# Performance work log

Hardware: AMD Instinct MI355X
Metric: run time of the kernel (lower is better)

Reference implementation:

```python
import jax, jax.numpy as jnp
import numpy as np

NUM_HEADS = 12
HEAD_DIM = 64
SCALE = HEAD_DIM ** -0.5


def setup_inputs() -> dict:
    key = jax.random.key(0)
    ks = jax.random.split(key, 5)
    B, N, C = 8, 1024, 768
    x = jax.random.normal(ks[0], (B, N, C), dtype=jnp.float32)
    qkv_w = jax.random.normal(ks[1], (3 * C, C), dtype=jnp.float32) * (C ** -0.5)
    qkv_b = jax.random.normal(ks[2], (3 * C,), dtype=jnp.float32) * 0.02
    proj_w = jax.random.normal(ks[3], (C, C), dtype=jnp.float32) * (C ** -0.5)
    proj_b = jax.random.normal(ks[4], (C,), dtype=jnp.float32) * 0.02
    return {"x": x, "qkv_w": qkv_w, "qkv_b": qkv_b, "proj_w": proj_w, "proj_b": proj_b}


def reference(x, qkv_w, qkv_b, proj_w, proj_b):
    B, N, C = x.shape
    H, D = NUM_HEADS, HEAD_DIM
    # qkv projection: (B,N,3C) -> (3,B,H,N,D)
    qkv = (x @ qkv_w.T + qkv_b).reshape(B, N, 3, H, D).transpose(2, 0, 3, 1, 4)
    q, k, v = qkv[0], qkv[1], qkv[2]
    q = q * SCALE
    # full N x N attention scores, softmax over keys
    attn = jax.nn.softmax(jnp.einsum("bhnd,bhmd->bhnm", q, k), axis=-1)
    # Libragrad: detach the softmax map before multiplying with V
    attn = jax.lax.stop_gradient(attn)
    out = jnp.einsum("bhnm,bhmd->bhnd", attn, v)  # (B,H,N,D)
    out = out.transpose(0, 2, 1, 3).reshape(B, N, C)
    return out @ proj_w.T + proj_b
```

## Files before the change

kernel.cpp:

```cpp
#include <hip/hip_runtime.h>

#define NH 12
#define HD 64
#define BB 8
#define SEQ 1024
#define CD 768

typedef __bf16 bf16x8 __attribute__((ext_vector_type(8)));
typedef float f32x4 __attribute__((ext_vector_type(4)));

__device__ __forceinline__ unsigned short f2bf(float f) {
    unsigned int u = __float_as_uint(f);
    u = (u + 0x7fffu + ((u >> 16) & 1u)) >> 16;
    return (unsigned short)u;
}

__device__ __forceinline__ void gld_lds16(const unsigned short* g, unsigned short* l) {
    __builtin_amdgcn_global_load_lds(
        (const __attribute__((address_space(1))) unsigned int*)g,
        (__attribute__((address_space(3))) unsigned int*)l, 16, 0, 0);
}

__device__ __forceinline__ int slot2key(int s) {
    return (s & 3) + 4 * ((s >> 3) & 3) + 16 * ((s >> 2) & 1) + 32 * (s >> 5);
}

#define N4_X 1572864
#define N4_W1 442368
#define N4_W2 147456
__global__ void cast_all(const float* __restrict__ x, const float* __restrict__ w1,
                         const float* __restrict__ w2,
                         unsigned short* __restrict__ ox, unsigned short* __restrict__ ow1,
                         unsigned short* __restrict__ ow2) {
    int i = blockIdx.x * blockDim.x + threadIdx.x;
    const float4* src;
    ushort4* dst;
    if (i < N4_X) {
        src = (const float4*)x + i; dst = (ushort4*)ox + i;
    } else if (i < N4_X + N4_W1) {
        src = (const float4*)w1 + (i - N4_X); dst = (ushort4*)ow1 + (i - N4_X);
    } else if (i < N4_X + N4_W1 + N4_W2) {
        src = (const float4*)w2 + (i - N4_X - N4_W1); dst = (ushort4*)ow2 + (i - N4_X - N4_W1);
    } else return;
    float4 f = *src;
    ushort4 o;
    o.x = f2bf(f.x); o.y = f2bf(f.y); o.z = f2bf(f.z); o.w = f2bf(f.w);
    *dst = o;
}

template<int MODE>
__global__ __launch_bounds__(256)
void gemm_bt(const unsigned short* __restrict__ A, const unsigned short* __restrict__ W,
             const float* __restrict__ bias,
             unsigned short* __restrict__ qb, unsigned short* __restrict__ kb,
             unsigned short* __restrict__ vb, float* __restrict__ fout,
             int M, int N, int K) {
    __shared__ __attribute__((aligned(16))) unsigned short As[128 * 32];
    __shared__ __attribute__((aligned(16))) unsigned short Bs[128 * 32];

    const int t    = threadIdx.x;
    const int bm0  = blockIdx.x * 128;
    const int bn0  = blockIdx.y * 128;
    const int wave = t >> 6;
    const int lane = t & 63;
    const int wm   = (wave >> 1) * 64;
    const int wn   = (wave & 1) * 64;
    const int col  = lane & 15;
    const int quad = lane >> 4;

    const int srow = t >> 2;
    const int scol = (t & 3) * 8;

    f32x4 acc[4][4];
#pragma unroll
    for (int i = 0; i < 4; i++)
#pragma unroll
        for (int j = 0; j < 4; j++) acc[i][j] = (f32x4){0.f, 0.f, 0.f, 0.f};

    for (int k0 = 0; k0 < K; k0 += 32) {
        __syncthreads();
        gld_lds16(A + (size_t)(bm0 + srow) * K + k0 + scol,      As + srow * 32 + scol);
        gld_lds16(A + (size_t)(bm0 + 64 + srow) * K + k0 + scol, As + (64 + srow) * 32 + scol);
        gld_lds16(W + (size_t)(bn0 + srow) * K + k0 + scol,      Bs + srow * 32 + scol);
        gld_lds16(W + (size_t)(bn0 + 64 + srow) * K + k0 + scol, Bs + (64 + srow) * 32 + scol);
        __syncthreads();

        bf16x8 af[4], bf[4];
#pragma unroll
        for (int mi = 0; mi < 4; mi++)
            af[mi] = *(const bf16x8*)(As + (wm + mi * 16 + col) * 32 + quad * 8);
#pragma unroll
        for (int ni = 0; ni < 4; ni++)
            bf[ni] = *(const bf16x8*)(Bs + (wn + ni * 16 + col) * 32 + quad * 8);
#pragma unroll
        for (int mi = 0; mi < 4; mi++)
#pragma unroll
            for (int ni = 0; ni < 4; ni++)
                acc[mi][ni] = __builtin_amdgcn_mfma_f32_16x16x32_bf16(
                    af[mi], bf[ni], acc[mi][ni], 0, 0, 0);
    }

    if (MODE == 1) {
#pragma unroll
        for (int mi = 0; mi < 4; mi++)
#pragma unroll
            for (int ni = 0; ni < 4; ni++) {
                const int n = bn0 + wn + ni * 16 + col;
                const float bv = bias[n];
#pragma unroll
                for (int r = 0; r < 4; r++) {
                    const int m = bm0 + wm + mi * 16 + quad * 4 + r;
                    fout[(size_t)m * N + n] = acc[mi][ni][r] + bv;
                }
            }
        return;
    }

    const int sel = bn0 / 768;
    const int nb  = bn0 - sel * 768;
    const int b   = bm0 >> 10;
    const int nqb = bm0 & 1023;
    unsigned short* const dstbuf = (sel == 0) ? qb : (sel == 1) ? kb : vb;
    const float scale = (sel == 0) ? 0.18033688f : 1.0f;

#pragma unroll
    for (int ni = 0; ni < 4; ni++) {
        const int hn = nb + wn + ni * 16;
        const int h  = hn >> 6;
        const int d0 = hn & 63;
        const float bv = bias[bn0 + wn + ni * 16 + col];
        unsigned short* const rowbase =
            dstbuf + ((size_t)(b * NH + h) * SEQ) * HD + d0 + col;
#pragma unroll
        for (int mi = 0; mi < 4; mi++)
#pragma unroll
            for (int r = 0; r < 4; r++) {
                const int nq = nqb + wm + mi * 16 + quad * 4 + r;
                rowbase[(size_t)nq * HD] = f2bf((acc[mi][ni][r] + bv) * scale);
            }
    }
}

__global__ __launch_bounds__(256)
void vtrans(const unsigned short* __restrict__ v, unsigned short* __restrict__ vt) {
    __shared__ __attribute__((aligned(16))) unsigned short T[64 * 72];
    const int bh = blockIdx.x;
    const int kt = blockIdx.y;
    const int t  = threadIdx.x;
    const int r  = t >> 2;
    const int c  = (t & 3) * 16;

    const unsigned short* src = v + ((size_t)bh * SEQ + kt * 64 + r) * HD + c;
    *(uint4*)(T + r * 72 + c)     = *(const uint4*)src;
    *(uint4*)(T + r * 72 + c + 8) = *(const uint4*)(src + 8);
    __syncthreads();

    union { unsigned short us[16]; uint4 u4[2]; } o;
#pragma unroll
    for (int j = 0; j < 16; j++) o.us[j] = T[slot2key(c + j) * 72 + r];
    unsigned short* dst = vt + ((size_t)bh * HD + r) * SEQ + kt * 64 + c;
    *(uint4*)dst       = o.u4[0];
    *(uint4*)(dst + 8) = o.u4[1];
}

__global__ __launch_bounds__(256, 6)
void attn_mfma(const unsigned short* __restrict__ qb,
               const unsigned short* __restrict__ kb,
               const unsigned short* __restrict__ vb,
               unsigned short* __restrict__ ob) {
    __shared__ __attribute__((aligned(16))) unsigned short Ks[64 * 72];
    __shared__ __attribute__((aligned(16))) unsigned short VT[64 * 72];

    const int t  = threadIdx.x;
    const int bh = blockIdx.x;
    const int qt = blockIdx.y;
    const size_t base = (size_t)bh * SEQ * HD;

    const int sr = t >> 2;
    const int sc = (t & 3) * 16;

    const int wave = t >> 6;
    const int lane = t & 63;
    const int col  = lane & 15;
    const int quad = lane >> 4;

    bf16x8 aq0, aq1;
    {
        const int q = qt * 64 + wave * 16 + col;
        aq0 = *(const bf16x8*)(qb + base + (size_t)q * HD + quad * 8);
        aq1 = *(const bf16x8*)(qb + base + (size_t)q * HD + 32 + quad * 8);
    }

    float l_r = 0.f;
    f32x4 accO[4];
#pragma unroll
    for (int di = 0; di < 4; di++) accO[di] = (f32x4){0.f, 0.f, 0.f, 0.f};

    const unsigned short* kp = kb + base + (size_t)sr * HD + sc;
    const unsigned short* vp = vb + base + (size_t)sr * SEQ + sc;
    uint4 kr0 = *(const uint4*)kp,  kr1 = *(const uint4*)(kp + 8);
    uint4 vr0 = *(const uint4*)vp,  vr1 = *(const uint4*)(vp + 8);

    for (int kc = 0; kc < 16; kc++) {
        __syncthreads();
        *(uint4*)(Ks + sr * 72 + sc)     = kr0;
        *(uint4*)(Ks + sr * 72 + sc + 8) = kr1;
        *(uint4*)(VT + sr * 72 + sc)     = vr0;
        *(uint4*)(VT + sr * 72 + sc + 8) = vr1;
        __syncthreads();

        if (kc < 15) {
            const unsigned short* kn = kp + (size_t)(kc + 1) * 64 * HD;
            const unsigned short* vn = vp + (size_t)(kc + 1) * 64;
            kr0 = *(const uint4*)kn; kr1 = *(const uint4*)(kn + 8);
            vr0 = *(const uint4*)vn; vr1 = *(const uint4*)(vn + 8);
        }

        f32x4 accT[4];
        __builtin_amdgcn_s_setprio(1);
#pragma unroll
        for (int ni = 0; ni < 4; ni++) {
            bf16x8 bk0 = *(const bf16x8*)(Ks + (ni * 16 + col) * 72 + quad * 8);
            bf16x8 bk1 = *(const bf16x8*)(Ks + (ni * 16 + col) * 72 + 32 + quad * 8);
            f32x4 z = (f32x4){0.f, 0.f, 0.f, 0.f};
            z = __builtin_amdgcn_mfma_f32_16x16x32_bf16(bk0, aq0, z, 0, 0, 0);
            z = __builtin_amdgcn_mfma_f32_16x16x32_bf16(bk1, aq1, z, 0, 0, 0);
            accT[ni] = z;
        }
        __builtin_amdgcn_s_setprio(0);

        union { __bf16 b[16]; bf16x8 v[2]; } apu;
#pragma unroll
        for (int ni = 0; ni < 4; ni++) {
            float p0 = __builtin_exp2f(accT[ni][0]);
            float p1 = __builtin_exp2f(accT[ni][1]);
            float p2 = __builtin_exp2f(accT[ni][2]);
            float p3 = __builtin_exp2f(accT[ni][3]);
            l_r += (p0 + p1) + (p2 + p3);
            apu.b[ni * 4 + 0] = (__bf16)p0;
            apu.b[ni * 4 + 1] = (__bf16)p1;
            apu.b[ni * 4 + 2] = (__bf16)p2;
            apu.b[ni * 4 + 3] = (__bf16)p3;
        }

        __builtin_amdgcn_s_setprio(1);
#pragma unroll
        for (int di = 0; di < 4; di++) {
            bf16x8 bv0 = *(const bf16x8*)(VT + (di * 16 + col) * 72 + quad * 8);
            bf16x8 bv1 = *(const bf16x8*)(VT + (di * 16 + col) * 72 + 32 + quad * 8);
            accO[di] = __builtin_amdgcn_mfma_f32_16x16x32_bf16(apu.v[0], bv0, accO[di], 0, 0, 0);
            accO[di] = __builtin_amdgcn_mfma_f32_16x16x32_bf16(apu.v[1], bv1, accO[di], 0, 0, 0);
        }
        __builtin_amdgcn_s_setprio(0);
    }

    const int b = bh / NH, h = bh - b * NH;
    float s = l_r;
    s += __shfl_xor(s, 16);
    s += __shfl_xor(s, 32);
#pragma unroll
    for (int r = 0; r < 4; r++) {
        const float inv = 1.f / __shfl(s, quad * 4 + r);
        const int q = qt * 64 + wave * 16 + quad * 4 + r;
        const size_t rowbase = ((size_t)b * SEQ + q) * CD + h * 64;
#pragma unroll
        for (int di = 0; di < 4; di++)
            ob[rowbase + di * 16 + col] = f2bf(accO[di][r] * inv);
    }
}

extern "C" void kernel_launch(void* const* d_in, const int* in_sizes, int n_in,
                              void* d_out, int out_size, void* d_ws, size_t ws_size,
                              hipStream_t stream) {
    const float* x      = (const float*)d_in[0];
    const float* qkv_w  = (const float*)d_in[1];
    const float* qkv_b  = (const float*)d_in[2];
    const float* proj_w = (const float*)d_in[3];
    const float* proj_b = (const float*)d_in[4];
    float* out = (float*)d_out;

    char* ws = (char*)d_ws;
    unsigned short* x_bf     = (unsigned short*)ws;
    unsigned short* qkvw_bf  = (unsigned short*)(ws + 12582912);
    unsigned short* projw_bf = (unsigned short*)(ws + 12582912 + 3538944);
    unsigned short* q_bf     = (unsigned short*)(ws + 12582912 + 3538944 + 1179648);
    unsigned short* k_bf     = q_bf + 6291456;
    unsigned short* v_bf     = k_bf + 6291456;
    unsigned short* vt_bf    = x_bf;
    unsigned short* attn_bf  = v_bf;

    cast_all<<<8448, 256, 0, stream>>>(x, qkv_w, proj_w, x_bf, qkvw_bf, projw_bf);

    gemm_bt<0><<<dim3(64, 18), 256, 0, stream>>>(x_bf, qkvw_bf, qkv_b,
                                                 q_bf, k_bf, v_bf, nullptr,
                                                 8192, 2304, 768);

    vtrans<<<dim3(96, 16), 256, 0, stream>>>(v_bf, vt_bf);

    attn_mfma<<<dim3(96, 16), 256, 0, stream>>>(q_bf, k_bf, vt_bf, attn_bf);

    gemm_bt<1><<<dim3(64, 6), 256, 0, stream>>>(attn_bf, projw_bf, proj_b,
                                                nullptr, nullptr, nullptr, out,
                                                8192, 768, 768);
}
```

Before: 213.1 us.

## Double-buffer K/V shared tiles in attention kernel to drop one barrier

```diff
diff --git a/kernel.cpp b/kernel.cpp
--- a/kernel.cpp
+++ b/kernel.cpp
@@ -163,13 +163,13 @@
     *(uint4*)(dst + 8) = o.u4[1];
 }
 
-__global__ __launch_bounds__(256, 6)
+__global__ __launch_bounds__(256, 4)
 void attn_mfma(const unsigned short* __restrict__ qb,
                const unsigned short* __restrict__ kb,
                const unsigned short* __restrict__ vb,
                unsigned short* __restrict__ ob) {
-    __shared__ __attribute__((aligned(16))) unsigned short Ks[64 * 72];
-    __shared__ __attribute__((aligned(16))) unsigned short VT[64 * 72];
+    __shared__ __attribute__((aligned(16))) unsigned short Ks[2][64 * 72];
+    __shared__ __attribute__((aligned(16))) unsigned short VT[2][64 * 72];
 
     const int t  = threadIdx.x;
     const int bh = blockIdx.x;
@@ -198,20 +198,29 @@
 
     const unsigned short* kp = kb + base + (size_t)sr * HD + sc;
     const unsigned short* vp = vb + base + (size_t)sr * SEQ + sc;
+    const int so = sr * 72 + sc;
+
     uint4 kr0 = *(const uint4*)kp,  kr1 = *(const uint4*)(kp + 8);
     uint4 vr0 = *(const uint4*)vp,  vr1 = *(const uint4*)(vp + 8);
-
-    for (int kc = 0; kc < 16; kc++) {
+    *(uint4*)(Ks[0] + so)     = kr0;
+    *(uint4*)(Ks[0] + so + 8) = kr1;
+    *(uint4*)(VT[0] + so)     = vr0;
+    *(uint4*)(VT[0] + so + 8) = vr1;
+    kr0 = *(const uint4*)(kp + 64 * HD);  kr1 = *(const uint4*)(kp + 64 * HD + 8);
+    vr0 = *(const uint4*)(vp + 64);       vr1 = *(const uint4*)(vp + 64 + 8);
+
+    auto chunk = [&](int kc, const unsigned short* Kc, const unsigned short* Vc,
+                     unsigned short* Kn, unsigned short* Vn) {
         __syncthreads();
-        *(uint4*)(Ks + sr * 72 + sc)     = kr0;
-        *(uint4*)(Ks + sr * 72 + sc + 8) = kr1;
-        *(uint4*)(VT + sr * 72 + sc)     = vr0;
-        *(uint4*)(VT + sr * 72 + sc + 8) = vr1;
-        __syncthreads();
-
         if (kc < 15) {
-            const unsigned short* kn = kp + (size_t)(kc + 1) * 64 * HD;
-            const unsigned short* vn = vp + (size_t)(kc + 1) * 64;
+            *(uint4*)(Kn + so)     = kr0;
+            *(uint4*)(Kn + so + 8) = kr1;
+            *(uint4*)(Vn + so)     = vr0;
+            *(uint4*)(Vn + so + 8) = vr1;
+        }
+        if (kc < 14) {
+            const unsigned short* kn = kp + (size_t)(kc + 2) * 64 * HD;
+            const unsigned short* vn = vp + (size_t)(kc + 2) * 64;
             kr0 = *(const uint4*)kn; kr1 = *(const uint4*)(kn + 8);
             vr0 = *(const uint4*)vn; vr1 = *(const uint4*)(vn + 8);
         }
@@ -220,8 +229,8 @@
         __builtin_amdgcn_s_setprio(1);
 #pragma unroll
         for (int ni = 0; ni < 4; ni++) {
-            bf16x8 bk0 = *(const bf16x8*)(Ks + (ni * 16 + col) * 72 + quad * 8);
-            bf16x8 bk1 = *(const bf16x8*)(Ks + (ni * 16 + col) * 72 + 32 + quad * 8);
+            bf16x8 bk0 = *(const bf16x8*)(Kc + (ni * 16 + col) * 72 + quad * 8);
+            bf16x8 bk1 = *(const bf16x8*)(Kc + (ni * 16 + col) * 72 + 32 + quad * 8);
             f32x4 z = (f32x4){0.f, 0.f, 0.f, 0.f};
             z = __builtin_amdgcn_mfma_f32_16x16x32_bf16(bk0, aq0, z, 0, 0, 0);
             z = __builtin_amdgcn_mfma_f32_16x16x32_bf16(bk1, aq1, z, 0, 0, 0);
@@ -246,12 +255,18 @@
         __builtin_amdgcn_s_setprio(1);
 #pragma unroll
         for (int di = 0; di < 4; di++) {
-            bf16x8 bv0 = *(const bf16x8*)(VT + (di * 16 + col) * 72 + quad * 8);
-            bf16x8 bv1 = *(const bf16x8*)(VT + (di * 16 + col) * 72 + 32 + quad * 8);
+            bf16x8 bv0 = *(const bf16x8*)(Vc + (di * 16 + col) * 72 + quad * 8);
+            bf16x8 bv1 = *(const bf16x8*)(Vc + (di * 16 + col) * 72 + 32 + quad * 8);
             accO[di] = __builtin_amdgcn_mfma_f32_16x16x32_bf16(apu.v[0], bv0, accO[di], 0, 0, 0);
             accO[di] = __builtin_amdgcn_mfma_f32_16x16x32_bf16(apu.v[1], bv1, accO[di], 0, 0, 0);
         }
         __builtin_amdgcn_s_setprio(0);
+    };
+
+#pragma unroll 1
+    for (int kc2 = 0; kc2 < 16; kc2 += 2) {
+        chunk(kc2,     Ks[0], VT[0], Ks[1], VT[1]);
+        chunk(kc2 + 1, Ks[1], VT[1], Ks[0], VT[0]);
     }
 
     const int b = bh / NH, h = bh - b * NH;
```

Measured after the change: 207.5 us. -2.6%, faster.
